# Kernel optimization log

Measured on AMD Instinct MI355X. Metric: run time of the kernel, lower is better.

The kernel has to match this reference:

```python
import jax, jax.numpy as jnp
import numpy as np

DIM = 512
HEADS = 8
DIM_HEAD = 64
INNER = HEADS * DIM_HEAD
SCALE = DIM_HEAD ** -0.5


def setup_inputs() -> dict:
    key = jax.random.key(0)
    k1, k2, k3, k4 = jax.random.split(key, 4)
    x = jax.random.normal(k1, (2, 4096, DIM), dtype=jnp.float32)
    # torch Linear stores weight [out, in]; we keep [in, out] for x @ W
    W_qkv = jax.random.normal(k2, (DIM, 3 * INNER), dtype=jnp.float32) * (DIM ** -0.5)
    W_out = jax.random.normal(k3, (INNER, DIM), dtype=jnp.float32) * (INNER ** -0.5)
    b_out = jax.random.normal(k4, (DIM,), dtype=jnp.float32) * 0.01
    return {"x": x, "W_qkv": W_qkv, "W_out": W_out, "b_out": b_out}


def reference(x, W_qkv, W_out, b_out):
    b, l, _ = x.shape
    qkv = x @ W_qkv  # [b, l, 3*inner]
    q, k, v = jnp.split(qkv, 3, axis=-1)

    def split_heads(t):  # [b, l, inner] -> [b, h, l, d]
        return t.reshape(b, l, HEADS, DIM_HEAD).transpose(0, 2, 1, 3)

    q, k, v = split_heads(q), split_heads(k), split_heads(v)
    attn = jnp.einsum('bhid,bhjd->bhij', q, k) * SCALE
    attn = jax.nn.softmax(attn, axis=-1)
    attned = jnp.einsum('bhij,bhjd->bhid', attn, v)
    attned = attned.transpose(0, 2, 1, 3).reshape(b, l, INNER)
    return attned @ W_out + b_out
```

## Files before the change

kernel.cpp:

```cpp
#include <hip/hip_runtime.h>
#include <hip/hip_bf16.h>

typedef short bf16x8 __attribute__((ext_vector_type(8)));
typedef float f32x4 __attribute__((ext_vector_type(4)));
typedef float f32x16 __attribute__((ext_vector_type(16)));
typedef unsigned uint2v __attribute__((ext_vector_type(2)));

#define MFMA16(a, b, c) __builtin_amdgcn_mfma_f32_16x16x32_bf16((a), (b), (c), 0, 0, 0)
#define MFMA32(a, b, c) __builtin_amdgcn_mfma_f32_32x32x16_bf16((a), (b), (c), 0, 0, 0)

__device__ __forceinline__ unsigned short f2bf(float f) {
    __hip_bfloat16 h = __float2bfloat16(f);
    return *reinterpret_cast<unsigned short*>(&h);
}
__device__ __forceinline__ unsigned pack2(float lo, float hi) {
    return (unsigned)f2bf(lo) | ((unsigned)f2bf(hi) << 16);
}
__device__ __forceinline__ uint2v plswap(unsigned a, unsigned b) {
    return __builtin_amdgcn_permlane32_swap(a, b, false, false);
}

__device__ __forceinline__ void gload_lds16(const unsigned short* g, unsigned short* l) {
    __builtin_amdgcn_global_load_lds(
        (const __attribute__((address_space(1))) void*)g,
        (__attribute__((address_space(3))) void*)l, 16, 0, 0);
}

__global__ __launch_bounds__(256) void k_cvt(const float* __restrict__ in,
                                             unsigned short* __restrict__ out, int n4) {
    int i = blockIdx.x * 256 + threadIdx.x;
    if (i < n4) {
        float4 v = reinterpret_cast<const float4*>(in)[i];
        ushort4 o;
        o.x = f2bf(v.x); o.y = f2bf(v.y); o.z = f2bf(v.z); o.w = f2bf(v.w);
        reinterpret_cast<ushort4*>(out)[i] = o;
    }
}

__global__ __launch_bounds__(256) void k_tr(const float* __restrict__ in,
                                            unsigned short* __restrict__ out, int R, int C) {
    __shared__ float t[64][65];
    int c0 = blockIdx.x * 64, r0 = blockIdx.y * 64;
    int lc = threadIdx.x & 63, lr4 = threadIdx.x >> 6;
#pragma unroll
    for (int j = 0; j < 16; ++j) {
        int r = lr4 + j * 4;
        t[r][lc] = in[(size_t)(r0 + r) * C + c0 + lc];
    }
    __syncthreads();
#pragma unroll
    for (int j = 0; j < 16; ++j) {
        int c = lr4 + j * 4;
        out[(size_t)(c0 + c) * R + r0 + lc] = f2bf(t[lc][c]);
    }
}

__device__ __forceinline__ void gemm_main_512(const unsigned short* __restrict__ A,
                                              const unsigned short* __restrict__ Bt,
                                              int m0, int n0,
                                              unsigned short* AL, unsigned short* BL,
                                              f32x4 acc[4][4]) {
    const int tid = threadIdx.x;
    const int lane = tid & 63, wid = tid >> 6;
    const int wr = wid >> 1, wc = wid & 1;
    const int lg = lane >> 4, lr = lane & 15;
    const int row0 = tid >> 2, c80 = (tid & 3) * 8;
    const int row1 = (tid + 256) >> 2, c81 = (tid & 3) * 8;

    for (int k0 = 0; k0 < 512; k0 += 32) {
        gload_lds16(&A[(size_t)(m0 + row0) * 512 + k0 + c80], &AL[tid * 8]);
        gload_lds16(&A[(size_t)(m0 + row1) * 512 + k0 + c81], &AL[(tid + 256) * 8]);
        gload_lds16(&Bt[(size_t)(n0 + row0) * 512 + k0 + c80], &BL[tid * 8]);
        gload_lds16(&Bt[(size_t)(n0 + row1) * 512 + k0 + c81], &BL[(tid + 256) * 8]);
        __syncthreads();
        bf16x8 af[4], bfr[4];
#pragma unroll
        for (int rt = 0; rt < 4; ++rt)
            af[rt] = *reinterpret_cast<const bf16x8*>(&AL[(wr * 64 + rt * 16 + lr) * 32 + lg * 8]);
#pragma unroll
        for (int ct = 0; ct < 4; ++ct)
            bfr[ct] = *reinterpret_cast<const bf16x8*>(&BL[(wc * 64 + ct * 16 + lr) * 32 + lg * 8]);
#pragma unroll
        for (int rt = 0; rt < 4; ++rt)
#pragma unroll
            for (int ct = 0; ct < 4; ++ct)
                acc[rt][ct] = MFMA16(af[rt], bfr[ct], acc[rt][ct]);
        __syncthreads();
    }
}

__global__ __launch_bounds__(256) void k_gemm_qkv(const unsigned short* __restrict__ X,
                                                  const unsigned short* __restrict__ Wt,
                                                  unsigned short* __restrict__ Qb,
                                                  unsigned short* __restrict__ Kb,
                                                  unsigned short* __restrict__ VbT) {
    __shared__ __align__(16) unsigned short AL[128 * 32];
    __shared__ __align__(16) unsigned short BL[128 * 32];
    f32x4 acc[4][4];
#pragma unroll
    for (int i = 0; i < 4; ++i)
#pragma unroll
        for (int j = 0; j < 4; ++j) acc[i][j] = (f32x4){0.f, 0.f, 0.f, 0.f};

    int m0 = blockIdx.x * 128, n0 = blockIdx.y * 128;
    gemm_main_512(X, Wt, m0, n0, AL, BL, acc);

    const int tid = threadIdx.x;
    const int lane = tid & 63, wid = tid >> 6;
    const int wr = wid >> 1, wc = wid & 1;
    const int lg = lane >> 4, lr = lane & 15;
    const int which = n0 >> 9;
#pragma unroll
    for (int rt = 0; rt < 4; ++rt) {
#pragma unroll
        for (int ct = 0; ct < 4; ++ct) {
            int col = n0 + wc * 64 + ct * 16 + lr;
            int inner = col & 511;
            int h = inner >> 6, d = inner & 63;
            int row0 = m0 + wr * 64 + rt * 16 + lg * 4;
            int b = row0 >> 12, l0 = row0 & 4095;
            if (which == 0) {
#pragma unroll
                for (int j = 0; j < 4; ++j)
                    Qb[(((size_t)(b * 8 + h)) * 4096 + l0 + j) * 64 + d] =
                        f2bf(acc[rt][ct][j] * 0.18033688f);
            } else if (which == 1) {
#pragma unroll
                for (int j = 0; j < 4; ++j)
                    Kb[(((size_t)(b * 8 + h)) * 4096 + l0 + j) * 64 + d] = f2bf(acc[rt][ct][j]);
            } else {
                ushort4 o;
                o.x = f2bf(acc[rt][ct][0]); o.y = f2bf(acc[rt][ct][1]);
                o.z = f2bf(acc[rt][ct][2]); o.w = f2bf(acc[rt][ct][3]);
                *reinterpret_cast<ushort4*>(
                    &VbT[(((size_t)(b * 8 + h)) * 64 + d) * 4096 + l0]) = o;
            }
        }
    }
}

__global__ __launch_bounds__(256) void k_gemm_out(const unsigned short* __restrict__ An,
                                                  const unsigned short* __restrict__ Wot,
                                                  const float* __restrict__ bout,
                                                  float* __restrict__ out) {
    __shared__ __align__(16) unsigned short AL[128 * 32];
    __shared__ __align__(16) unsigned short BL[128 * 32];
    f32x4 acc[4][4];
#pragma unroll
    for (int i = 0; i < 4; ++i)
#pragma unroll
        for (int j = 0; j < 4; ++j) acc[i][j] = (f32x4){0.f, 0.f, 0.f, 0.f};

    int m0 = blockIdx.x * 128, n0 = blockIdx.y * 128;
    gemm_main_512(An, Wot, m0, n0, AL, BL, acc);

    const int tid = threadIdx.x;
    const int lane = tid & 63, wid = tid >> 6;
    const int wr = wid >> 1, wc = wid & 1;
    const int lg = lane >> 4, lr = lane & 15;
#pragma unroll
    for (int rt = 0; rt < 4; ++rt) {
#pragma unroll
        for (int ct = 0; ct < 4; ++ct) {
            int col = n0 + wc * 64 + ct * 16 + lr;
            float bv = bout[col];
#pragma unroll
            for (int j = 0; j < 4; ++j) {
                int row = m0 + wr * 64 + rt * 16 + lg * 4 + j;
                out[(size_t)row * 512 + col] = acc[rt][ct][j] + bv;
            }
        }
    }
}

__global__ __launch_bounds__(256) void k_attn(const unsigned short* __restrict__ Q,
                                              const unsigned short* __restrict__ K,
                                              const unsigned short* __restrict__ VT,
                                              unsigned short* __restrict__ An) {
    __shared__ __align__(16) unsigned short KL[64 * 72];
    __shared__ __align__(16) unsigned short VTl[64 * 72];

    const int flat = blockIdx.x;
    const int bh = flat & 15;
    const int qt = flat >> 4;
    const size_t base = (size_t)bh * 4096 * 64;
    const int tid = threadIdx.x, lane = tid & 63, wid = tid >> 6;
    const int l31 = lane & 31, hi = lane >> 5;
    const int q0 = qt * 128 + wid * 32;

    bf16x8 qf[4];
#pragma unroll
    for (int i = 0; i < 4; ++i)
        qf[i] = *reinterpret_cast<const bf16x8*>(
            &Q[base + (size_t)(q0 + l31) * 64 + i * 16 + hi * 8]);

    f32x16 oacc[2];
    f32x16 sacc;
#pragma unroll
    for (int r = 0; r < 16; ++r) { oacc[0][r] = 0.f; oacc[1][r] = 0.f; sacc[r] = 0.f; }

    bf16x8 ones;
#pragma unroll
    for (int j = 0; j < 8; ++j) ones[j] = (short)0x3F80;

    const int r0 = tid >> 3, c0 = (tid & 7) * 8;

    bf16x8 kreg[2], vreg[2];
#pragma unroll
    for (int i = 0; i < 2; ++i) {
        kreg[i] = *reinterpret_cast<const bf16x8*>(&K[base + (size_t)(r0 + i * 32) * 64 + c0]);
        vreg[i] = *reinterpret_cast<const bf16x8*>(&VT[base + (size_t)(r0 + i * 32) * 4096 + c0]);
    }
#pragma unroll
    for (int i = 0; i < 2; ++i) {
        *reinterpret_cast<bf16x8*>(&KL[(r0 + i * 32) * 72 + c0]) = kreg[i];
        *reinterpret_cast<bf16x8*>(&VTl[(r0 + i * 32) * 72 + c0]) = vreg[i];
    }
    __syncthreads();

    for (int kv = 0; kv < 64; ++kv) {
        const int kv0n = kv * 64 + 64;
        if (kv < 63) {
#pragma unroll
            for (int i = 0; i < 2; ++i) {
                kreg[i] = *reinterpret_cast<const bf16x8*>(
                    &K[base + (size_t)(kv0n + r0 + i * 32) * 64 + c0]);
                vreg[i] = *reinterpret_cast<const bf16x8*>(
                    &VT[base + (size_t)(r0 + i * 32) * 4096 + kv0n + c0]);
            }
        }

        f32x16 s[2];
#pragma unroll
        for (int r = 0; r < 16; ++r) { s[0][r] = 0.f; s[1][r] = 0.f; }
        __builtin_amdgcn_s_setprio(1);
#pragma unroll
        for (int t = 0; t < 2; ++t) {
#pragma unroll
            for (int i = 0; i < 4; ++i) {
                bf16x8 kf = *reinterpret_cast<const bf16x8*>(
                    &KL[(t * 32 + l31) * 72 + i * 16 + hi * 8]);
                s[t] = MFMA32(kf, qf[i], s[t]);
            }
        }
        __builtin_amdgcn_s_setprio(0);

        bf16x8 pa[2][2];
#pragma unroll
        for (int t = 0; t < 2; ++t) {
            unsigned pk[8];
#pragma unroll
            for (int p = 0; p < 8; ++p)
                pk[p] = pack2(__builtin_amdgcn_exp2f(s[t][2 * p]),
                              __builtin_amdgcn_exp2f(s[t][2 * p + 1]));
            uint2v s02 = plswap(pk[0], pk[2]);
            uint2v s13 = plswap(pk[1], pk[3]);
            uint2v s46 = plswap(pk[4], pk[6]);
            uint2v s57 = plswap(pk[5], pk[7]);
            union { unsigned u[4]; bf16x8 v; } w0, w1;
            w0.u[0] = s02.x; w0.u[1] = s13.x; w0.u[2] = s02.y; w0.u[3] = s13.y;
            w1.u[0] = s46.x; w1.u[1] = s57.x; w1.u[2] = s46.y; w1.u[3] = s57.y;
            pa[t][0] = w0.v;
            pa[t][1] = w1.v;
        }

        __builtin_amdgcn_s_setprio(1);
#pragma unroll
        for (int t = 0; t < 2; ++t) {
#pragma unroll
            for (int half = 0; half < 2; ++half) {
                const int m = 2 * t + half;
                sacc = MFMA32(pa[t][half], ones, sacc);
#pragma unroll
                for (int dt = 0; dt < 2; ++dt) {
                    bf16x8 vf = *reinterpret_cast<const bf16x8*>(
                        &VTl[(dt * 32 + l31) * 72 + m * 16 + hi * 8]);
                    oacc[dt] = MFMA32(pa[t][half], vf, oacc[dt]);
                }
            }
        }
        __builtin_amdgcn_s_setprio(0);

        __syncthreads();
        if (kv < 63) {
#pragma unroll
            for (int i = 0; i < 2; ++i) {
                *reinterpret_cast<bf16x8*>(&KL[(r0 + i * 32) * 72 + c0]) = kreg[i];
                *reinterpret_cast<bf16x8*>(&VTl[(r0 + i * 32) * 72 + c0]) = vreg[i];
            }
        }
        __syncthreads();
    }

    const int b = bh >> 3, h = bh & 7;
#pragma unroll
    for (int reg = 0; reg < 16; ++reg) {
        float inv = 1.f / sacc[reg];
        int row = q0 + (reg & 3) + 8 * (reg >> 2) + 4 * hi;
#pragma unroll
        for (int dt = 0; dt < 2; ++dt) {
            int d = dt * 32 + l31;
            An[((size_t)b * 4096 + row) * 512 + h * 64 + d] = f2bf(oacc[dt][reg] * inv);
        }
    }
}

extern "C" void kernel_launch(void* const* d_in, const int* in_sizes, int n_in,
                              void* d_out, int out_size, void* d_ws, size_t ws_size,
                              hipStream_t stream) {
    const float* x    = (const float*)d_in[0];
    const float* Wqkv = (const float*)d_in[1];
    const float* Wout = (const float*)d_in[2];
    const float* bout = (const float*)d_in[3];
    float* out = (float*)d_out;

    char* ws = (char*)d_ws;
    unsigned short* Xbf  = (unsigned short*)(ws);
    unsigned short* Wqkt = (unsigned short*)(ws + 8388608);
    unsigned short* Wot  = (unsigned short*)(ws + 8388608 + 1572864);
    unsigned short* Qb   = (unsigned short*)(ws + 10485760);
    unsigned short* Kb   = (unsigned short*)(ws + 18874368);
    unsigned short* VbT  = (unsigned short*)(ws + 27262976);
    unsigned short* An   = (unsigned short*)(ws + 35651584);

    k_cvt<<<4096, 256, 0, stream>>>(x, Xbf, 4194304 / 4);
    k_tr<<<dim3(24, 8), 256, 0, stream>>>(Wqkv, Wqkt, 512, 1536);
    k_tr<<<dim3(8, 8), 256, 0, stream>>>(Wout, Wot, 512, 512);
    k_gemm_qkv<<<dim3(64, 12), 256, 0, stream>>>(Xbf, Wqkt, Qb, Kb, VbT);
    k_attn<<<dim3(512), 256, 0, stream>>>(Qb, Kb, VbT, An);
    k_gemm_out<<<dim3(64, 4), 256, 0, stream>>>(An, Wot, bout, out);
}
```

Before: 208.8 us.

## Split attention KV range across two blocks, add reduce kernel, merge prep kernels

The attention kernel now launches a second grid dimension, so each block processes half of the 4096 keys. It writes unnormalized bf16 partial outputs and per-row softmax denominators, and a new reduce kernel sums the two halves and normalizes. This doubles the block count from 512 to 1024 for better CU occupancy. It costs extra global traffic for the partials, one more launch, and some precision from storing unnormalized partials in bf16. Separately, the input convert and the two weight transposes are fused into one prep kernel to cut launch overhead.

```diff
diff --git a/kernel.cpp b/kernel.cpp
--- a/kernel.cpp
+++ b/kernel.cpp
@@ -13,6 +13,10 @@
     __hip_bfloat16 h = __float2bfloat16(f);
     return *reinterpret_cast<unsigned short*>(&h);
 }
+__device__ __forceinline__ float bf2f(unsigned short s) {
+    union { unsigned u; float f; } v; v.u = (unsigned)s << 16;
+    return v.f;
+}
 __device__ __forceinline__ unsigned pack2(float lo, float hi) {
     return (unsigned)f2bf(lo) | ((unsigned)f2bf(hi) << 16);
 }
@@ -26,21 +30,10 @@
         (__attribute__((address_space(3))) void*)l, 16, 0, 0);
 }
 
-__global__ __launch_bounds__(256) void k_cvt(const float* __restrict__ in,
-                                             unsigned short* __restrict__ out, int n4) {
-    int i = blockIdx.x * 256 + threadIdx.x;
-    if (i < n4) {
-        float4 v = reinterpret_cast<const float4*>(in)[i];
-        ushort4 o;
-        o.x = f2bf(v.x); o.y = f2bf(v.y); o.z = f2bf(v.z); o.w = f2bf(v.w);
-        reinterpret_cast<ushort4*>(out)[i] = o;
-    }
-}
-
-__global__ __launch_bounds__(256) void k_tr(const float* __restrict__ in,
-                                            unsigned short* __restrict__ out, int R, int C) {
-    __shared__ float t[64][65];
-    int c0 = blockIdx.x * 64, r0 = blockIdx.y * 64;
+__device__ __forceinline__ void tr_block(const float* __restrict__ in,
+                                         unsigned short* __restrict__ out,
+                                         int R, int C, int bx, int by, float (*t)[65]) {
+    int c0 = bx * 64, r0 = by * 64;
     int lc = threadIdx.x & 63, lr4 = threadIdx.x >> 6;
 #pragma unroll
     for (int j = 0; j < 16; ++j) {
@@ -52,6 +45,29 @@
     for (int j = 0; j < 16; ++j) {
         int c = lr4 + j * 4;
         out[(size_t)(c0 + c) * R + r0 + lc] = f2bf(t[lc][c]);
+    }
+}
+
+__global__ __launch_bounds__(256) void k_prep(const float* __restrict__ x,
+                                              unsigned short* __restrict__ Xbf,
+                                              const float* __restrict__ Wqkv,
+                                              unsigned short* __restrict__ Wqkt,
+                                              const float* __restrict__ Wout,
+                                              unsigned short* __restrict__ Wot) {
+    __shared__ float t[64][65];
+    int bid = blockIdx.x;
+    if (bid < 4096) {
+        int i = bid * 256 + threadIdx.x;
+        float4 v = reinterpret_cast<const float4*>(x)[i];
+        ushort4 o;
+        o.x = f2bf(v.x); o.y = f2bf(v.y); o.z = f2bf(v.z); o.w = f2bf(v.w);
+        reinterpret_cast<ushort4*>(Xbf)[i] = o;
+    } else if (bid < 4096 + 192) {
+        int idx = bid - 4096;
+        tr_block(Wqkv, Wqkt, 512, 1536, idx % 24, idx / 24, t);
+    } else {
+        int idx = bid - 4288;
+        tr_block(Wout, Wot, 512, 512, idx % 8, idx / 8, t);
     }
 }
 
@@ -176,13 +192,17 @@
 __global__ __launch_bounds__(256) void k_attn(const unsigned short* __restrict__ Q,
                                               const unsigned short* __restrict__ K,
                                               const unsigned short* __restrict__ VT,
-                                              unsigned short* __restrict__ An) {
+                                              unsigned short* __restrict__ Op0,
+                                              unsigned short* __restrict__ Op1,
+                                              float* __restrict__ Lp) {
     __shared__ __align__(16) unsigned short KL[64 * 72];
     __shared__ __align__(16) unsigned short VTl[64 * 72];
 
     const int flat = blockIdx.x;
     const int bh = flat & 15;
     const int qt = flat >> 4;
+    const int hh = blockIdx.y;
+    const int kvbase = hh * 2048;
     const size_t base = (size_t)bh * 4096 * 64;
     const int tid = threadIdx.x, lane = tid & 63, wid = tid >> 6;
     const int l31 = lane & 31, hi = lane >> 5;
@@ -208,8 +228,10 @@
     bf16x8 kreg[2], vreg[2];
 #pragma unroll
     for (int i = 0; i < 2; ++i) {
-        kreg[i] = *reinterpret_cast<const bf16x8*>(&K[base + (size_t)(r0 + i * 32) * 64 + c0]);
-        vreg[i] = *reinterpret_cast<const bf16x8*>(&VT[base + (size_t)(r0 + i * 32) * 4096 + c0]);
+        kreg[i] = *reinterpret_cast<const bf16x8*>(
+            &K[base + (size_t)(kvbase + r0 + i * 32) * 64 + c0]);
+        vreg[i] = *reinterpret_cast<const bf16x8*>(
+            &VT[base + (size_t)(r0 + i * 32) * 4096 + kvbase + c0]);
     }
 #pragma unroll
     for (int i = 0; i < 2; ++i) {
@@ -218,9 +240,9 @@
     }
     __syncthreads();
 
-    for (int kv = 0; kv < 64; ++kv) {
-        const int kv0n = kv * 64 + 64;
-        if (kv < 63) {
+    for (int kv = 0; kv < 32; ++kv) {
+        const int kv0n = kvbase + kv * 64 + 64;
+        if (kv < 31) {
 #pragma unroll
             for (int i = 0; i < 2; ++i) {
                 kreg[i] = *reinterpret_cast<const bf16x8*>(
@@ -282,7 +304,7 @@
         __builtin_amdgcn_s_setprio(0);
 
         __syncthreads();
-        if (kv < 63) {
+        if (kv < 31) {
 #pragma unroll
             for (int i = 0; i < 2; ++i) {
                 *reinterpret_cast<bf16x8*>(&KL[(r0 + i * 32) * 72 + c0]) = kreg[i];
@@ -292,17 +314,40 @@
         __syncthreads();
     }
 
+    unsigned short* Op = hh ? Op1 : Op0;
     const int b = bh >> 3, h = bh & 7;
 #pragma unroll
     for (int reg = 0; reg < 16; ++reg) {
-        float inv = 1.f / sacc[reg];
         int row = q0 + (reg & 3) + 8 * (reg >> 2) + 4 * hi;
 #pragma unroll
         for (int dt = 0; dt < 2; ++dt) {
             int d = dt * 32 + l31;
-            An[((size_t)b * 4096 + row) * 512 + h * 64 + d] = f2bf(oacc[dt][reg] * inv);
-        }
-    }
+            Op[((size_t)b * 4096 + row) * 512 + h * 64 + d] = f2bf(oacc[dt][reg]);
+        }
+        if (l31 == 0)
+            Lp[((size_t)(hh * 16 + bh)) * 4096 + row] = sacc[reg];
+    }
+}
+
+__global__ __launch_bounds__(256) void k_reduce(const unsigned short* __restrict__ O0,
+                                                const unsigned short* __restrict__ O1,
+                                                const float* __restrict__ Lp,
+                                                unsigned short* __restrict__ An) {
+    int i4 = blockIdx.x * 256 + threadIdx.x;
+    int e = i4 * 4;
+    int r = e >> 9;
+    int c = e & 511, h = c >> 6;
+    int b = r >> 12, l = r & 4095;
+    int lidx = (b * 8 + h) * 4096 + l;
+    float inv = 1.f / (Lp[lidx] + Lp[16 * 4096 + lidx]);
+    ushort4 a = *reinterpret_cast<const ushort4*>(&O0[e]);
+    ushort4 bq = *reinterpret_cast<const ushort4*>(&O1[e]);
+    ushort4 o;
+    o.x = f2bf((bf2f(a.x) + bf2f(bq.x)) * inv);
+    o.y = f2bf((bf2f(a.y) + bf2f(bq.y)) * inv);
+    o.z = f2bf((bf2f(a.z) + bf2f(bq.z)) * inv);
+    o.w = f2bf((bf2f(a.w) + bf2f(bq.w)) * inv);
+    *reinterpret_cast<ushort4*>(&An[e]) = o;
 }
 
 extern "C" void kernel_launch(void* const* d_in, const int* in_sizes, int n_in,
@@ -322,11 +367,13 @@
     unsigned short* Kb   = (unsigned short*)(ws + 18874368);
     unsigned short* VbT  = (unsigned short*)(ws + 27262976);
     unsigned short* An   = (unsigned short*)(ws + 35651584);
-
-    k_cvt<<<4096, 256, 0, stream>>>(x, Xbf, 4194304 / 4);
-    k_tr<<<dim3(24, 8), 256, 0, stream>>>(Wqkv, Wqkt, 512, 1536);
-    k_tr<<<dim3(8, 8), 256, 0, stream>>>(Wout, Wot, 512, 512);
+    unsigned short* Op0  = Xbf;
+    unsigned short* Op1  = An;
+    float*          Lp   = (float*)(ws + 8388608);
+
+    k_prep<<<4352, 256, 0, stream>>>(x, Xbf, Wqkv, Wqkt, Wout, Wot);
     k_gemm_qkv<<<dim3(64, 12), 256, 0, stream>>>(Xbf, Wqkt, Qb, Kb, VbT);
-    k_attn<<<dim3(512), 256, 0, stream>>>(Qb, Kb, VbT, An);
+    k_attn<<<dim3(512, 2), 256, 0, stream>>>(Qb, Kb, VbT, Op0, Op1, Lp);
+    k_reduce<<<4096, 256, 0, stream>>>(Op0, Op1, Lp, An);
     k_gemm_out<<<dim3(64, 4), 256, 0, stream>>>(An, Wot, bout, out);
 }
```

After: 210.2 us. No clear change (+0.6%).
